# Kernel tuning notes

Measured on AMD Instinct MI355X. Metric: run time of the kernel, lower is better.

Reference implementation:

```python
import jax, jax.numpy as jnp
import numpy as np

DIM = 384; HEADS = 12; HD = DIM // HEADS; WS = 7; SHIFT = 3
RES = (14, 14, 14); N = WS ** 3; HID = 4 * DIM
NW = (RES[0] // WS) * (RES[1] // WS) * (RES[2] // WS)


def _np_attn_mask():
    Z, H, W = RES
    img = np.zeros((Z, H, W), np.float32)
    sl = (slice(0, -WS), slice(-WS, -SHIFT), slice(-SHIFT, None))
    cnt = 0
    for z in sl:
        for h in sl:
            for w in sl:
                img[z, h, w] = cnt
                cnt += 1
    m = img.reshape(Z // WS, WS, H // WS, WS, W // WS, WS)
    m = m.transpose(0, 2, 4, 1, 3, 5).reshape(NW, N)
    d = m[:, None, :] - m[:, :, None]
    return np.where(d != 0, -100.0, 0.0).astype(np.float32)  # [NW, N, N]


def _np_cpb_table_and_index():
    # continuous relative coords table, log-spaced (SwinV2), pretrained_window_size=0 -> normalize by WS-1
    r = np.arange(-(WS - 1), WS, dtype=np.float32)
    g = np.stack(np.meshgrid(r, r, r, indexing='ij'), -1)
    g = g / (WS - 1) * 8.0
    g = np.sign(g) * np.log2(np.abs(g) + 1.0) / np.log2(8.0)
    table = g.reshape(-1, 3)  # [(2W-1)^3, 3]
    c = np.stack(np.meshgrid(np.arange(WS), np.arange(WS), np.arange(WS), indexing='ij'))
    c = c.reshape(3, -1)  # [3, N]
    rel = c[:, :, None] - c[:, None, :] + (WS - 1)
    S = 2 * WS - 1
    idx = rel[0] * S * S + rel[1] * S + rel[2]  # [N, N]
    return table.astype(np.float32), idx.astype(np.int32)

_ATTN_MASK = _np_attn_mask()
_CPB_TABLE, _REL_IDX = _np_cpb_table_and_index()


def _ln(x, g, b, eps=1e-5):
    m = jnp.mean(x, -1, keepdims=True)
    v = jnp.mean(jnp.square(x - m), -1, keepdims=True)
    return (x - m) * jax.lax.rsqrt(v + eps) * g + b


def _win_part(x):  # [B,Z,H,W,C] -> [B*NW, WS,WS,WS, C]
    B, Z, H, W, C = x.shape
    x = x.reshape(B, Z // WS, WS, H // WS, WS, W // WS, WS, C)
    return x.transpose(0, 1, 3, 5, 2, 4, 6, 7).reshape(-1, WS, WS, WS, C)


def _win_rev(w, B):  # [B*NW, WS,WS,WS, C] -> [B,Z,H,W,C]
    Z, H, W = RES
    x = w.reshape(B, Z // WS, H // WS, W // WS, WS, WS, WS, -1)
    return x.transpose(0, 1, 4, 2, 5, 3, 6, 7).reshape(B, Z, H, W, -1)


def _forward(x, qkv_w, q_bias, v_bias, logit_scale, cpb_w1, cpb_b1, cpb_w2,
             proj_w, proj_b, norm1_g, norm1_b, norm2_g, norm2_b,
             fc1_w, fc1_b, fc2_w, fc2_b):
    Z, H, W = RES
    B, L, C = x.shape
    shortcut = x
    xg = x.reshape(B, Z, H, W, C)
    xg = jnp.roll(xg, (-SHIFT, -SHIFT, -SHIFT), axis=(1, 2, 3))
    xw = _win_part(xg).reshape(-1, N, C)  # [B*NW, N, C]

    qkv_b = jnp.concatenate([q_bias, jnp.zeros_like(q_bias), v_bias])
    qkv = xw @ qkv_w.T + qkv_b
    qkv = qkv.reshape(-1, N, 3, HEADS, HD).transpose(2, 0, 3, 1, 4)
    q, k, v = qkv[0], qkv[1], qkv[2]  # [B*NW, HEADS, N, HD]

    qn = q / jnp.maximum(jnp.linalg.norm(q, axis=-1, keepdims=True), 1e-12)
    kn = k / jnp.maximum(jnp.linalg.norm(k, axis=-1, keepdims=True), 1e-12)
    scale = jnp.exp(jnp.minimum(logit_scale, np.log(100.0)))  # [HEADS,1,1]
    attn = jnp.einsum('whnd,whmd->whnm', qn, kn) * scale

    # continuous relative position bias
    tbl = jax.nn.relu(jnp.asarray(_CPB_TABLE) @ cpb_w1.T + cpb_b1) @ cpb_w2.T  # [(2W-1)^3, HEADS]
    bias = 16.0 * jax.nn.sigmoid(tbl[_REL_IDX])  # [N, N, HEADS]
    attn = attn + bias.transpose(2, 0, 1)[None]

    mask = jnp.asarray(_ATTN_MASK)  # [NW, N, N]
    attn = attn.reshape(B, NW, HEADS, N, N) + mask[None, :, None]
    attn = jax.nn.softmax(attn.reshape(-1, HEADS, N, N), axis=-1)

    out = jnp.einsum('whnm,whmd->whnd', attn, v)
    out = out.transpose(0, 2, 1, 3).reshape(-1, N, C)
    out = out @ proj_w.T + proj_b

    xg = _win_rev(out.reshape(-1, WS, WS, WS, C), B)
    xg = jnp.roll(xg, (SHIFT, SHIFT, SHIFT), axis=(1, 2, 3))
    xa = xg.reshape(B, L, C)

    x1 = shortcut + _ln(xa, norm1_g, norm1_b)
    h = jax.nn.gelu(x1 @ fc1_w.T + fc1_b, approximate=False) @ fc2_w.T + fc2_b
    return x1 + _ln(h, norm2_g, norm2_b)


def setup_inputs() -> dict:
    key = jax.random.key(0)
    ks = jax.random.split(key, 8)
    B, L = 8, RES[0] * RES[1] * RES[2]
    s = 0.02
    return {
        'x': jax.random.normal(ks[0], (B, L, DIM), jnp.float32),
        'qkv_w': jax.random.normal(ks[1], (3 * DIM, DIM), jnp.float32) * s,
        'q_bias': jnp.zeros((DIM,), jnp.float32),
        'v_bias': jnp.zeros((DIM,), jnp.float32),
        'logit_scale': jnp.full((HEADS, 1, 1), np.log(10.0), jnp.float32),
        'cpb_w1': jax.random.normal(ks[2], (512, 3), jnp.float32) * s,
        'cpb_b1': jnp.zeros((512,), jnp.float32),
        'cpb_w2': jax.random.normal(ks[3], (HEADS, 512), jnp.float32) * s,
        'proj_w': jax.random.normal(ks[4], (DIM, DIM), jnp.float32) * s,
        'proj_b': jnp.zeros((DIM,), jnp.float32),
        'norm1_g': jnp.ones((DIM,), jnp.float32),
        'norm1_b': jnp.zeros((DIM,), jnp.float32),
        'norm2_g': jnp.ones((DIM,), jnp.float32),
        'norm2_b': jnp.zeros((DIM,), jnp.float32),
        'fc1_w': jax.random.normal(ks[5], (HID, DIM), jnp.float32) * s,
        'fc1_b': jnp.zeros((HID,), jnp.float32),
        'fc2_w': jax.random.normal(ks[6], (DIM, HID), jnp.float32) * s,
        'fc2_b': jnp.zeros((DIM,), jnp.float32),
    }


def reference(x, qkv_w, q_bias, v_bias, logit_scale, cpb_w1, cpb_b1, cpb_w2,
              proj_w, proj_b, norm1_g, norm1_b, norm2_g, norm2_b,
              fc1_w, fc1_b, fc2_w, fc2_b):
    return _forward(x, qkv_w, q_bias, v_bias, logit_scale, cpb_w1, cpb_b1, cpb_w2,
                    proj_w, proj_b, norm1_g, norm1_b, norm2_g, norm2_b,
                    fc1_w, fc1_b, fc2_w, fc2_b)
```

## Files before the change

### kernel.cpp

```cpp
#include <hip/hip_runtime.h>
#include <hip/hip_bf16.h>
#include <stdint.h>

namespace {

typedef __attribute__((ext_vector_type(8))) short s8v;
typedef __attribute__((ext_vector_type(4))) short s4v;
typedef __attribute__((ext_vector_type(4))) float f4v;
typedef __attribute__((ext_vector_type(8))) unsigned short us8;

constexpr int kN = 343;
constexpr size_t kPlaneE = 768ull * 343 * 32;
constexpr int kM = 21952;
constexpr float kL2E = 1.44269504f;

__device__ __forceinline__ int regionOf(int c) { return c < 7 ? 0 : (c < 11 ? 1 : 2); }

__device__ __forceinline__ int winRowMap(int wtok) {
  int w = wtok / kN, nn = wtok % kN;
  int bb = w >> 3, nwi = w & 7;
  int nz = nn / 49, nh = (nn / 7) % 7, nw = nn % 7;
  int uz = (((nwi >> 2) & 1) * 7 + nz + 3) % 14;
  int uh = (((nwi >> 1) & 1) * 7 + nh + 3) % 14;
  int uw = (((nwi     ) & 1) * 7 + nw + 3) % 14;
  return bb * 2744 + uz * 196 + uh * 14 + uw;
}

__device__ __forceinline__ unsigned short f2bf(float f) {
  union { float f; unsigned u; } a; a.f = f;
  unsigned r = a.u + 0x7fffu + ((a.u >> 16) & 1u);
  return (unsigned short)(r >> 16);
}
__device__ __forceinline__ float bf2f(unsigned short u) {
  union { unsigned u; float f; } a; a.u = ((unsigned)u) << 16; return a.f;
}
__device__ __forceinline__ unsigned cvtpk(float lo, float hi) {
  unsigned r;
  asm("v_cvt_pk_bf16_f32 %0, %1, %2" : "=v"(r) : "v"(lo), "v"(hi));
  return r;
}
__device__ __forceinline__ float fexp2(float x) {
#if __has_builtin(__builtin_amdgcn_exp2f)
  return __builtin_amdgcn_exp2f(x);
#else
  return exp2f(x);
#endif
}

#if __has_builtin(__builtin_amdgcn_mfma_f32_16x16x16bf16_1k)
__device__ __forceinline__ f4v mfma16(s4v a, s4v b, f4v c) {
  return __builtin_amdgcn_mfma_f32_16x16x16bf16_1k(a, b, c, 0, 0, 0);
}
#else
__device__ __forceinline__ f4v mfma16(s4v a, s4v b, f4v c) {
  f4v d;
  asm("v_mfma_f32_16x16x16_bf16 %0, %1, %2, %3" : "=v"(d) : "v"(a), "v"(b), "v"(c));
  return d;
}
#endif

__device__ __forceinline__ void gload16(const void* g, void* l) {
  __builtin_amdgcn_global_load_lds(
      (const __attribute__((address_space(1))) unsigned int*)g,
      (__attribute__((address_space(3))) unsigned int*)l, 16, 0, 0);
}

__device__ __forceinline__ float cpbFeat(int i) {
  float v = (float)(i - 6) * (8.0f / 6.0f);
  float a = log2f(fabsf(v) + 1.0f) * (1.0f / 3.0f);
  return v < 0.0f ? -a : a;
}

__global__ __launch_bounds__(256) void cvt_bf16_kernel(
    const float* __restrict__ src, unsigned short* __restrict__ dst, int n8) {
  int i = blockIdx.x * 256 + threadIdx.x;
  if (i >= n8) return;
  const float* s = src + (size_t)i * 8;
  float4 a = *(const float4*)s;
  float4 b = *(const float4*)(s + 4);
  us8 o;
  o[0]=f2bf(a.x); o[1]=f2bf(a.y); o[2]=f2bf(a.z); o[3]=f2bf(a.w);
  o[4]=f2bf(b.x); o[5]=f2bf(b.y); o[6]=f2bf(b.z); o[7]=f2bf(b.w);
  *(us8*)(dst + (size_t)i * 8) = o;
}

__global__ __launch_bounds__(256) void gather_x_kernel(
    const float* __restrict__ x, unsigned short* __restrict__ xg) {
  int chunk = blockIdx.x * 256 + threadIdx.x;
  if (chunk >= kM * 48) return;
  int wtok = chunk / 48, c = (chunk - wtok * 48) * 8;
  long row = winRowMap(wtok);
  const float* s = x + row * 384 + c;
  float4 a = *(const float4*)s;
  float4 b = *(const float4*)(s + 4);
  us8 o;
  o[0]=f2bf(a.x); o[1]=f2bf(a.y); o[2]=f2bf(a.z); o[3]=f2bf(a.w);
  o[4]=f2bf(b.x); o[5]=f2bf(b.y); o[6]=f2bf(b.z); o[7]=f2bf(b.w);
  *(us8*)(xg + (size_t)wtok * 384 + c) = o;
}

__global__ __launch_bounds__(256) void cpb_table_kernel(
    const float* __restrict__ w1, const float* __restrict__ b1,
    const float* __restrict__ w2, float* __restrict__ tbl) {
  int t = blockIdx.x * 256 + threadIdx.x;
  if (t >= 2197 * 12) return;
  int row = t / 12, h = t - (t / 12) * 12;
  float f0 = cpbFeat(row / 169), f1 = cpbFeat((row / 13) % 13), f2 = cpbFeat(row % 13);
  float acc = 0.f;
  for (int j = 0; j < 512; ++j) {
    float hid = fmaf(f0, w1[j*3+0], fmaf(f1, w1[j*3+1], fmaf(f2, w1[j*3+2], b1[j])));
    hid = fmaxf(hid, 0.f);
    acc = fmaf(hid, w2[h*512 + j], acc);
  }
  tbl[row * 12 + h] = acc;
}

__global__ __launch_bounds__(256) void cpb_bias_frag_kernel(
    const float* __restrict__ tbl, float* __restrict__ biasf) {
  int gid = blockIdx.x * 256 + threadIdx.x;
  if (gid >= 12 * 22 * 22 * 64) return;
  int lane = gid & 63, tile = gid >> 6;
  int jt = tile % 22, qt = (tile / 22) % 22, h = tile / 484;
  int i = qt * 16 + (lane & 15);
  int j0 = jt * 16 + ((lane >> 4) << 2);
  float v[4];
  #pragma unroll
  for (int r = 0; r < 4; ++r) {
    int j = j0 + r;
    float val = -43000.f;
    if (i < kN && j < kN) {
      int iz = i/49, ih = (i/7)%7, iw = i%7;
      int jz = j/49, jh = (j/7)%7, jw = j%7;
      int idx = (iz-jz+6)*169 + (ih-jh+6)*13 + (iw-jw+6);
      float tv = tbl[idx*12 + h];
      val = (16.f / (1.f + __expf(-tv))) * kL2E;
    }
    v[r] = val;
  }
  *(float4*)(biasf + ((size_t)tile << 8) + (lane << 2)) = make_float4(v[0], v[1], v[2], v[3]);
}

__global__ __launch_bounds__(256) void qknorm_kernel(
    unsigned short* __restrict__ qp, unsigned short* __restrict__ kp,
    const float* __restrict__ ls) {
  int gid = blockIdx.x * 256 + threadIdx.x;
  if (gid >= 768 * kN) return;
  int wh = gid / kN, t = gid - (gid / kN) * kN;
  int h = wh % 12;
  unsigned short* qr = qp + (size_t)wh * kN * 32 + (size_t)t * 32;
  unsigned short* kr = kp + (size_t)wh * kN * 32 + (size_t)t * 32;
  us8 q[4], k[4];
  float qs = 0.f, ks = 0.f;
  #pragma unroll
  for (int c = 0; c < 4; ++c) {
    q[c] = *(const us8*)(qr + c * 8);
    k[c] = *(const us8*)(kr + c * 8);
    #pragma unroll
    for (int e = 0; e < 8; ++e) {
      float fq = bf2f(q[c][e]); qs = fmaf(fq, fq, qs);
      float fk = bf2f(k[c][e]); ks = fmaf(fk, fk, ks);
    }
  }
  float qm = rsqrtf(fmaxf(qs, 1e-24f)) * __expf(fminf(ls[h], 4.6051702f)) * kL2E;
  float km = rsqrtf(fmaxf(ks, 1e-24f));
  #pragma unroll
  for (int c = 0; c < 4; ++c) {
    us8 oq, ok;
    #pragma unroll
    for (int e = 0; e < 8; ++e) {
      oq[e] = f2bf(bf2f(q[c][e]) * qm);
      ok[e] = f2bf(bf2f(k[c][e]) * km);
    }
    *(us8*)(qr + c * 8) = oq;
    *(us8*)(kr + c * 8) = ok;
  }
}

template <int MODE>
__global__ __launch_bounds__(256) void gemm_bf16(
    const unsigned short* __restrict__ A, const unsigned short* __restrict__ W,
    const float* __restrict__ b0, const float* __restrict__ b1,
    void* __restrict__ outv, int K, int N) {
  __shared__ __align__(16) unsigned short As[2][128][32];
  __shared__ __align__(16) unsigned short Bs[2][128][32];
  const int tid = threadIdx.x, lane = tid & 63, wid = tid >> 6;
  const int wr = wid >> 1, wc = wid & 1;
  const int lq = lane & 15, gq = lane >> 4;
  const int m0 = blockIdx.y * 128, n0 = blockIdx.x * 128;

  const int r0 = tid >> 2, c0 = (tid & 3) << 3;
  const unsigned short* gA0 = A + (size_t)(m0 + r0) * K + c0;
  const unsigned short* gA1 = A + (size_t)(m0 + 64 + r0) * K + c0;
  const unsigned short* gB0 = W + (size_t)(n0 + r0) * K + c0;
  const unsigned short* gB1 = W + (size_t)(n0 + 64 + r0) * K + c0;

  f4v acc[4][4];
  const f4v zero4 = {0.f, 0.f, 0.f, 0.f};
  #pragma unroll
  for (int i = 0; i < 4; ++i)
    #pragma unroll
    for (int j = 0; j < 4; ++j) acc[i][j] = zero4;

  const int nk = K >> 5;
#define STAGE(buf, kt)                                         \
  gload16(gA0 + (kt) * 32, &As[buf][r0][c0]);                  \
  gload16(gA1 + (kt) * 32, &As[buf][64 + r0][c0]);             \
  gload16(gB0 + (kt) * 32, &Bs[buf][r0][c0]);                  \
  gload16(gB1 + (kt) * 32, &Bs[buf][64 + r0][c0]);

  STAGE(0, 0);
  __syncthreads();
  for (int kt = 0; kt < nk; ++kt) {
    int cur = kt & 1;
    if (kt + 1 < nk) { STAGE(cur ^ 1, kt + 1); }
    s8v af[4];
    #pragma unroll
    for (int mt = 0; mt < 4; ++mt)
      af[mt] = *(const s8v*)&As[cur][wr * 64 + mt * 16 + lq][gq * 8];
    #pragma unroll
    for (int nt = 0; nt < 4; ++nt) {
      s8v bfr = *(const s8v*)&Bs[cur][wc * 64 + nt * 16 + lq][gq * 8];
      #pragma unroll
      for (int mt = 0; mt < 4; ++mt)
        acc[mt][nt] = __builtin_amdgcn_mfma_f32_16x16x32_bf16(af[mt], bfr, acc[mt][nt], 0, 0, 0);
    }
    __syncthreads();
  }
#undef STAGE

  if (MODE == 0) {
    unsigned short* qkv = (unsigned short*)outv;
    #pragma unroll
    for (int nt = 0; nt < 4; ++nt) {
      int cg = n0 + wc * 64 + nt * 16 + lq;
      int which = cg / 384, rem = cg - which * 384;
      const float* bp = (which == 0) ? b0 : (which == 2 ? b1 : nullptr);
      float badd = bp ? bp[rem] : 0.f;
      unsigned short* plane = qkv + (size_t)which * kPlaneE;
      #pragma unroll
      for (int mt = 0; mt < 4; ++mt)
        #pragma unroll
        for (int r = 0; r < 4; ++r) {
          int mg = m0 + wr * 64 + mt * 16 + gq * 4 + r;
          if (mg < kM) {
            int w = mg / kN, nn = mg - (mg / kN) * kN;
            plane[((size_t)(w * 12 + (rem >> 5)) * kN + nn) * 32 + (rem & 31)] =
                f2bf(acc[mt][nt][r] + badd);
          }
        }
    }
  } else {
    #pragma unroll
    for (int nt = 0; nt < 4; ++nt) {
      int cg = n0 + wc * 64 + nt * 16 + lq;
      float badd = b0[cg];
      #pragma unroll
      for (int mt = 0; mt < 4; ++mt)
        #pragma unroll
        for (int r = 0; r < 4; ++r) {
          size_t mg = (size_t)(m0 + wr * 64 + mt * 16 + gq * 4 + r);
          float t = acc[mt][nt][r] + badd;
          if (MODE == 2) {
            t = 0.5f * t * (1.f + erff(t * 0.70710678118f));
            ((unsigned short*)outv)[mg * N + cg] = f2bf(t);
          } else {
            ((float*)outv)[mg * N + cg] = t;
          }
        }
    }
  }
}

__global__ __launch_bounds__(512) void attn_mfma(
    const unsigned short* __restrict__ qp, const unsigned short* __restrict__ kp,
    const unsigned short* __restrict__ vp, const float* __restrict__ biasf,
    unsigned short* __restrict__ outb) {
  __shared__ __align__(16) unsigned short Ksh[352][40];
  __shared__ __align__(16) unsigned short Vt[32][364];
  __shared__ float cntS[352];

  const int bid = blockIdx.x;
  const int h = bid >> 6, w = bid & 63;
  const int wh = w * 12 + h;
  const int nwi = w & 7;
  const int tid = threadIdx.x, lane = tid & 63, wid = tid >> 6;
  const int lq = lane & 15, gq = lane >> 4;
  const unsigned short* qb = qp + (size_t)wh * kN * 32;
  const unsigned short* kb = kp + (size_t)wh * kN * 32;
  const unsigned short* vb = vp + (size_t)wh * kN * 32;

  for (int idx = tid; idx < 1408; idx += 512) {
    int r = idx >> 2, c8 = (idx & 3) << 3;
    us8 v = {0, 0, 0, 0, 0, 0, 0, 0};
    if (r < kN) v = *(const us8*)(kb + r * 32 + c8);
    *(us8*)&Ksh[r][c8] = v;
  }
  for (int idx = tid; idx < 288; idx += 512)
    Vt[idx / 9][343 + (idx % 9)] = 0;
  for (int idx = tid; idx < 1372; idx += 512) {
    int r = idx >> 2, c8 = (idx & 3) << 3;
    us8 v = *(const us8*)(vb + r * 32 + c8);
    #pragma unroll
    for (int e = 0; e < 8; ++e) Vt[c8 + e][r] = v[e];
  }
  if (tid < 352) {
    int t = tid;
    if (t < kN) {
      int jz = t / 49, jh = (t / 7) % 7, jw = t % 7;
      cntS[t] = (float)(regionOf(((nwi >> 2) & 1) * 7 + jz) * 9 +
                        regionOf(((nwi >> 1) & 1) * 7 + jh) * 3 +
                        regionOf(((nwi     ) & 1) * 7 + jw));
    } else {
      cntS[t] = 0.f;
    }
  }
  __syncthreads();

  const f4v zero4 = {0.f, 0.f, 0.f, 0.f};

  for (int qt = wid; qt < 22; qt += 8) {
    const int i0 = qt * 16;
    s8v qa = *(const s8v*)(qb + (size_t)(i0 + lq) * 32 + gq * 8);
    float ci = cntS[i0 + lq];
    const float* bb = biasf + (((size_t)(h * 22 + qt) * 22) << 8) + (lane << 2);

    float l2[22][4];
    #pragma unroll
    for (int jt = 0; jt < 22; ++jt) {
      s8v kf = *(const s8v*)&Ksh[jt * 16 + lq][gq * 8];
      f4v s4 = __builtin_amdgcn_mfma_f32_16x16x32_bf16(kf, qa, zero4, 0, 0, 0);
      float bqa[4];
      *(float4*)bqa = *(const float4*)(bb + ((size_t)jt << 8));
      #pragma unroll
      for (int r = 0; r < 4; ++r) {
        float cj = cntS[jt * 16 + 4 * gq + r];
        l2[jt][r] = s4[r] + bqa[r] + ((cj != ci) ? -144.269504f : 0.f);
      }
    }
    float m = -3e38f;
    #pragma unroll
    for (int jt = 0; jt < 22; ++jt)
      m = fmaxf(m, fmaxf(fmaxf(l2[jt][0], l2[jt][1]), fmaxf(l2[jt][2], l2[jt][3])));
    m = fmaxf(m, __shfl_xor(m, 16));
    m = fmaxf(m, __shfl_xor(m, 32));
    float sum = 0.f;
    s4v pa[22];
    #pragma unroll
    for (int jt = 0; jt < 22; ++jt) {
      float p0 = fexp2(l2[jt][0] - m), p1 = fexp2(l2[jt][1] - m);
      float p2 = fexp2(l2[jt][2] - m), p3 = fexp2(l2[jt][3] - m);
      sum += (p0 + p1) + (p2 + p3);
      union { unsigned u[2]; s4v s; } pk;
      pk.u[0] = cvtpk(p0, p1);
      pk.u[1] = cvtpk(p2, p3);
      pa[jt] = pk.s;
    }
    sum += __shfl_xor(sum, 16);
    sum += __shfl_xor(sum, 32);
    float rinv = 1.f / sum;

    f4v o0 = zero4, o1 = zero4;
    #pragma unroll
    for (int jt = 0; jt < 22; ++jt) {
      s4v v0 = *(const s4v*)&Vt[lq][jt * 16 + 4 * gq];
      s4v v1 = *(const s4v*)&Vt[16 + lq][jt * 16 + 4 * gq];
      o0 = mfma16(pa[jt], v0, o0);
      o1 = mfma16(pa[jt], v1, o1);
    }
    asm volatile("s_nop 7\ns_nop 7" :::);
    #pragma unroll
    for (int r = 0; r < 4; ++r) {
      int q = i0 + 4 * gq + r;
      float rv = __shfl(rinv, 4 * gq + r);
      if (q < kN) {
        size_t base = ((size_t)(w * kN + q)) * 384 + h * 32;
        outb[base + lq]      = f2bf(o0[r] * rv);
        outb[base + 16 + lq] = f2bf(o1[r] * rv);
      }
    }
  }
}

template <int GATHER, int WBF>
__global__ __launch_bounds__(256) void ln_kernel(
    const float* __restrict__ src, const float* __restrict__ resid,
    const float* __restrict__ g, const float* __restrict__ b,
    float* __restrict__ out, unsigned short* __restrict__ outbf) {
  int row = blockIdx.x * 4 + (threadIdx.x >> 6), lane = threadIdx.x & 63;
  long dst = GATHER ? (long)winRowMap(row) : (long)row;
  float t[6];
  float sum = 0.f, sq = 0.f;
  #pragma unroll
  for (int i = 0; i < 6; ++i) {
    t[i] = src[(long)row * 384 + i * 64 + lane];
    sum += t[i];
    sq = fmaf(t[i], t[i], sq);
  }
  #pragma unroll
  for (int o = 32; o; o >>= 1) { sum += __shfl_xor(sum, o); sq += __shfl_xor(sq, o); }
  float mean = sum * (1.f / 384.f);
  float var = sq * (1.f / 384.f) - mean * mean;
  float rs = rsqrtf(var + 1e-5f);
  #pragma unroll
  for (int i = 0; i < 6; ++i) {
    int c = i * 64 + lane;
    float val = resid[dst * 384 + c] + (t[i] - mean) * rs * g[c] + b[c];
    out[dst * 384 + c] = val;
    if (WBF) outbf[dst * 384 + c] = f2bf(val);
  }
}

}

extern "C" void kernel_launch(void* const* d_in, const int* in_sizes, int n_in,
                              void* d_out, int out_size, void* d_ws, size_t ws_size,
                              hipStream_t stream) {
  const float* x      = (const float*)d_in[0];
  const float* qkv_w  = (const float*)d_in[1];
  const float* q_bias = (const float*)d_in[2];
  const float* v_bias = (const float*)d_in[3];
  const float* lscale = (const float*)d_in[4];
  const float* cpb_w1 = (const float*)d_in[5];
  const float* cpb_b1 = (const float*)d_in[6];
  const float* cpb_w2 = (const float*)d_in[7];
  const float* proj_w = (const float*)d_in[8];
  const float* proj_b = (const float*)d_in[9];
  const float* n1g    = (const float*)d_in[10];
  const float* n1b    = (const float*)d_in[11];
  const float* n2g    = (const float*)d_in[12];
  const float* n2b    = (const float*)d_in[13];
  const float* fc1_w  = (const float*)d_in[14];
  const float* fc1_b  = (const float*)d_in[15];
  const float* fc2_w  = (const float*)d_in[16];
  const float* fc2_b  = (const float*)d_in[17];
  float* outp = (float*)d_out;
  char* wsb = (char*)d_ws;

  float*          biasf = (float*)(wsb + 0);
  float*          tbl   = (float*)(wsb + 5947392);
  unsigned short* qkvp  = (unsigned short*)(wsb + 6052864);
  unsigned short* xg    = (unsigned short*)(wsb + 56630272);
  unsigned short* attno = (unsigned short*)(wsb + 73538560);
  unsigned short* wts   = (unsigned short*)(wsb + 90446848);
  float*          projt = (float*)(wsb + 93985792);
  float*          x1    = (float*)(wsb + 127802368);
  unsigned short* x1b   = (unsigned short*)(wsb + 161520640);
  unsigned short* hbuf  = qkvp;
  float*          h2    = projt;

  unsigned short* wq  = wts;
  unsigned short* wpj = wts + 442368;
  unsigned short* wf1 = wts + 589824;
  unsigned short* wf2 = wts + 1179648;

  cvt_bf16_kernel<<<216, 256, 0, stream>>>(qkv_w, wq, 55296);
  cvt_bf16_kernel<<<72,  256, 0, stream>>>(proj_w, wpj, 18432);
  cvt_bf16_kernel<<<288, 256, 0, stream>>>(fc1_w, wf1, 73728);
  cvt_bf16_kernel<<<288, 256, 0, stream>>>(fc2_w, wf2, 73728);
  gather_x_kernel<<<4116, 256, 0, stream>>>(x, xg);
  cpb_table_kernel<<<103, 256, 0, stream>>>(cpb_w1, cpb_b1, cpb_w2, tbl);
  cpb_bias_frag_kernel<<<1452, 256, 0, stream>>>(tbl, biasf);

  gemm_bf16<0><<<dim3(9, 172), 256, 0, stream>>>(xg, wq, q_bias, v_bias, qkvp, 384, 1152);

  qknorm_kernel<<<1029, 256, 0, stream>>>(qkvp, qkvp + kPlaneE, lscale);

  attn_mfma<<<768, 512, 0, stream>>>(qkvp, qkvp + kPlaneE, qkvp + 2 * kPlaneE, biasf, attno);

  gemm_bf16<1><<<dim3(3, 172), 256, 0, stream>>>(attno, wpj, proj_b, nullptr, projt, 384, 384);

  ln_kernel<1, 1><<<5488, 256, 0, stream>>>(projt, x, n1g, n1b, x1, x1b);

  gemm_bf16<2><<<dim3(12, 172), 256, 0, stream>>>(x1b, wf1, fc1_b, nullptr, hbuf, 384, 1536);

  gemm_bf16<1><<<dim3(3, 172), 256, 0, stream>>>(hbuf, wf2, fc2_b, nullptr, h2, 1536, 384);

  ln_kernel<0, 0><<<5488, 256, 0, stream>>>(h2, x1, n2g, n2b, outp, nullptr);
}
```

Baseline: 411.4 us.

## Store intermediates in bf16, swizzle GEMM blocks across XCDs, merge weight converts

```diff
diff --git a/kernel.cpp b/kernel.cpp
--- a/kernel.cpp
+++ b/kernel.cpp
@@ -71,17 +71,30 @@
   return v < 0.0f ? -a : a;
 }
 
-__global__ __launch_bounds__(256) void cvt_bf16_kernel(
-    const float* __restrict__ src, unsigned short* __restrict__ dst, int n8) {
+__device__ __forceinline__ int xcdSwz(int bid, int nwg) {
+  int q = nwg >> 3, r = nwg & 7;
+  int x = bid & 7, p = bid >> 3;
+  return (x < r ? x * (q + 1) : r * (q + 1) + (x - r) * q) + p;
+}
+
+__global__ __launch_bounds__(256) void cvt_all_kernel(
+    const float* __restrict__ qkv_w, const float* __restrict__ proj_w,
+    const float* __restrict__ fc1_w, const float* __restrict__ fc2_w,
+    unsigned short* __restrict__ wts) {
   int i = blockIdx.x * 256 + threadIdx.x;
-  if (i >= n8) return;
-  const float* s = src + (size_t)i * 8;
+  if (i >= 221184) return;
+  const float* src; size_t dstoff; int rel;
+  if (i < 55296)       { src = qkv_w;  rel = i;          dstoff = 0; }
+  else if (i < 73728)  { src = proj_w; rel = i - 55296;  dstoff = 442368; }
+  else if (i < 147456) { src = fc1_w;  rel = i - 73728;  dstoff = 589824; }
+  else                 { src = fc2_w;  rel = i - 147456; dstoff = 1179648; }
+  const float* s = src + (size_t)rel * 8;
   float4 a = *(const float4*)s;
   float4 b = *(const float4*)(s + 4);
   us8 o;
   o[0]=f2bf(a.x); o[1]=f2bf(a.y); o[2]=f2bf(a.z); o[3]=f2bf(a.w);
   o[4]=f2bf(b.x); o[5]=f2bf(b.y); o[6]=f2bf(b.z); o[7]=f2bf(b.w);
-  *(us8*)(dst + (size_t)i * 8) = o;
+  *(us8*)(wts + dstoff + (size_t)rel * 8) = o;
 }
 
 __global__ __launch_bounds__(256) void gather_x_kernel(
@@ -180,13 +193,15 @@
 __global__ __launch_bounds__(256) void gemm_bf16(
     const unsigned short* __restrict__ A, const unsigned short* __restrict__ W,
     const float* __restrict__ b0, const float* __restrict__ b1,
-    void* __restrict__ outv, int K, int N) {
+    unsigned short* __restrict__ outv, int K, int N, int nbx) {
   __shared__ __align__(16) unsigned short As[2][128][32];
   __shared__ __align__(16) unsigned short Bs[2][128][32];
+  const int wg = xcdSwz(blockIdx.x, gridDim.x);
+  const int by = wg / nbx, bx = wg - by * nbx;
+  const int m0 = by * 128, n0 = bx * 128;
   const int tid = threadIdx.x, lane = tid & 63, wid = tid >> 6;
   const int wr = wid >> 1, wc = wid & 1;
   const int lq = lane & 15, gq = lane >> 4;
-  const int m0 = blockIdx.y * 128, n0 = blockIdx.x * 128;
 
   const int r0 = tid >> 2, c0 = (tid & 3) << 3;
   const unsigned short* gA0 = A + (size_t)(m0 + r0) * K + c0;
@@ -229,14 +244,13 @@
 #undef STAGE
 
   if (MODE == 0) {
-    unsigned short* qkv = (unsigned short*)outv;
     #pragma unroll
     for (int nt = 0; nt < 4; ++nt) {
       int cg = n0 + wc * 64 + nt * 16 + lq;
       int which = cg / 384, rem = cg - which * 384;
       const float* bp = (which == 0) ? b0 : (which == 2 ? b1 : nullptr);
       float badd = bp ? bp[rem] : 0.f;
-      unsigned short* plane = qkv + (size_t)which * kPlaneE;
+      unsigned short* plane = outv + (size_t)which * kPlaneE;
       #pragma unroll
       for (int mt = 0; mt < 4; ++mt)
         #pragma unroll
@@ -260,12 +274,8 @@
         for (int r = 0; r < 4; ++r) {
           size_t mg = (size_t)(m0 + wr * 64 + mt * 16 + gq * 4 + r);
           float t = acc[mt][nt][r] + badd;
-          if (MODE == 2) {
-            t = 0.5f * t * (1.f + erff(t * 0.70710678118f));
-            ((unsigned short*)outv)[mg * N + cg] = f2bf(t);
-          } else {
-            ((float*)outv)[mg * N + cg] = t;
-          }
+          if (MODE == 2) t = 0.5f * t * (1.f + erff(t * 0.70710678118f));
+          outv[mg * N + cg] = f2bf(t);
         }
     }
   }
@@ -381,18 +391,18 @@
   }
 }
 
-template <int GATHER, int WBF>
+template <int GATHER, int RB, int OB>
 __global__ __launch_bounds__(256) void ln_kernel(
-    const float* __restrict__ src, const float* __restrict__ resid,
+    const unsigned short* __restrict__ src, const void* __restrict__ residv,
     const float* __restrict__ g, const float* __restrict__ b,
-    float* __restrict__ out, unsigned short* __restrict__ outbf) {
+    float* __restrict__ outf, unsigned short* __restrict__ outb) {
   int row = blockIdx.x * 4 + (threadIdx.x >> 6), lane = threadIdx.x & 63;
   long dst = GATHER ? (long)winRowMap(row) : (long)row;
   float t[6];
   float sum = 0.f, sq = 0.f;
   #pragma unroll
   for (int i = 0; i < 6; ++i) {
-    t[i] = src[(long)row * 384 + i * 64 + lane];
+    t[i] = bf2f(src[(long)row * 384 + i * 64 + lane]);
     sum += t[i];
     sq = fmaf(t[i], t[i], sq);
   }
@@ -404,9 +414,11 @@
   #pragma unroll
   for (int i = 0; i < 6; ++i) {
     int c = i * 64 + lane;
-    float val = resid[dst * 384 + c] + (t[i] - mean) * rs * g[c] + b[c];
-    out[dst * 384 + c] = val;
-    if (WBF) outbf[dst * 384 + c] = f2bf(val);
+    float rv = RB ? bf2f(((const unsigned short*)residv)[dst * 384 + c])
+                  : ((const float*)residv)[dst * 384 + c];
+    float val = rv + (t[i] - mean) * rs * g[c] + b[c];
+    if (OB) outb[dst * 384 + c] = f2bf(val);
+    else    outf[dst * 384 + c] = val;
   }
 }
 
@@ -442,38 +454,34 @@
   unsigned short* xg    = (unsigned short*)(wsb + 56630272);
   unsigned short* attno = (unsigned short*)(wsb + 73538560);
   unsigned short* wts   = (unsigned short*)(wsb + 90446848);
-  float*          projt = (float*)(wsb + 93985792);
-  float*          x1    = (float*)(wsb + 127802368);
-  unsigned short* x1b   = (unsigned short*)(wsb + 161520640);
+  unsigned short* projt = (unsigned short*)(wsb + 93985792);
+  unsigned short* x1b   = (unsigned short*)(wsb + 110894080);
   unsigned short* hbuf  = qkvp;
-  float*          h2    = projt;
+  unsigned short* h2    = projt;
 
   unsigned short* wq  = wts;
   unsigned short* wpj = wts + 442368;
   unsigned short* wf1 = wts + 589824;
   unsigned short* wf2 = wts + 1179648;
 
-  cvt_bf16_kernel<<<216, 256, 0, stream>>>(qkv_w, wq, 55296);
-  cvt_bf16_kernel<<<72,  256, 0, stream>>>(proj_w, wpj, 18432);
-  cvt_bf16_kernel<<<288, 256, 0, stream>>>(fc1_w, wf1, 73728);
-  cvt_bf16_kernel<<<288, 256, 0, stream>>>(fc2_w, wf2, 73728);
+  cvt_all_kernel<<<864, 256, 0, stream>>>(qkv_w, proj_w, fc1_w, fc2_w, wts);
   gather_x_kernel<<<4116, 256, 0, stream>>>(x, xg);
   cpb_table_kernel<<<103, 256, 0, stream>>>(cpb_w1, cpb_b1, cpb_w2, tbl);
   cpb_bias_frag_kernel<<<1452, 256, 0, stream>>>(tbl, biasf);
 
-  gemm_bf16<0><<<dim3(9, 172), 256, 0, stream>>>(xg, wq, q_bias, v_bias, qkvp, 384, 1152);
+  gemm_bf16<0><<<1548, 256, 0, stream>>>(xg, wq, q_bias, v_bias, qkvp, 384, 1152, 9);
 
   qknorm_kernel<<<1029, 256, 0, stream>>>(qkvp, qkvp + kPlaneE, lscale);
 
   attn_mfma<<<768, 512, 0, stream>>>(qkvp, qkvp + kPlaneE, qkvp + 2 * kPlaneE, biasf, attno);
 
-  gemm_bf16<1><<<dim3(3, 172), 256, 0, stream>>>(attno, wpj, proj_b, nullptr, projt, 384, 384);
-
-  ln_kernel<1, 1><<<5488, 256, 0, stream>>>(projt, x, n1g, n1b, x1, x1b);
-
-  gemm_bf16<2><<<dim3(12, 172), 256, 0, stream>>>(x1b, wf1, fc1_b, nullptr, hbuf, 384, 1536);
-
-  gemm_bf16<1><<<dim3(3, 172), 256, 0, stream>>>(hbuf, wf2, fc2_b, nullptr, h2, 1536, 384);
-
-  ln_kernel<0, 0><<<5488, 256, 0, stream>>>(h2, x1, n2g, n2b, outp, nullptr);
-}
+  gemm_bf16<1><<<516, 256, 0, stream>>>(attno, wpj, proj_b, nullptr, projt, 384, 384, 3);
+
+  ln_kernel<1, 0, 1><<<5488, 256, 0, stream>>>(projt, x, n1g, n1b, nullptr, x1b);
+
+  gemm_bf16<2><<<2064, 256, 0, stream>>>(x1b, wf1, fc1_b, nullptr, hbuf, 384, 1536, 12);
+
+  gemm_bf16<1><<<516, 256, 0, stream>>>(hbuf, wf2, fc2_b, nullptr, h2, 1536, 384, 3);
+
+  ln_kernel<0, 1, 0><<<5488, 256, 0, stream>>>(h2, x1b, n2g, n2b, outp, nullptr);
+}
```

After: 368.8 us. -10.3%, faster.
